# Kernel tuning notes

Hardware: AMD Instinct MI355X
Metric: run time of the kernel (lower is better)

The kernel has to match this reference:

```python
import jax, jax.numpy as jnp
import numpy as np

N, A, B, C = 256, 1024, 64, 16


def setup_inputs() -> dict:
    key = jax.random.key(0)
    k1, k2, k3 = jax.random.split(key, 3)
    x = jax.random.normal(k1, (N, A), dtype=jnp.float32)
    weight = jax.random.normal(k2, (A, B * C), dtype=jnp.float32) * 0.02
    bias = jax.random.normal(k3, (B,), dtype=jnp.float32) * 0.02
    return {"x": x, "weight": weight, "bias": bias}


def reference(x, weight, bias):
    # x: [N, A]; weight: [A, B*C]; bias: [B]
    n = x.shape[0]
    mat = (x @ weight).reshape(n, B, C)              # [N, B, C]
    # pairwise L1 over the C (kernel) axis -> [N, N, B]
    l1 = jnp.abs(mat[:, None, :, :] - mat[None, :, :, :]).sum(axis=-1)
    # exp(-L1), sum over the first (broadcast) axis as in the torch code,
    # which includes the self term exp(0)=1
    out = jnp.exp(-l1).sum(axis=0) + bias            # [N, B]
    return out
```

## Files before the change

### kernel.cpp

```cpp
#include <hip/hip_runtime.h>

#define LOG2E 1.4426950408889634f

typedef __bf16 bf16x8 __attribute__((ext_vector_type(8)));
typedef float  f32x4  __attribute__((ext_vector_type(4)));

__device__ inline unsigned short f2bf(float f){
  unsigned u = __float_as_uint(f);
  unsigned r = u + 0x7FFFu + ((u >> 16) & 1u);
  return (unsigned short)(r >> 16);
}
__device__ inline unsigned pack2(float lo, float hi){
  return (unsigned)f2bf(lo) | ((unsigned)f2bf(hi) << 16);
}

__global__ __launch_bounds__(256) void k_gemm_fused(const float* __restrict__ X,
                                                    const float* __restrict__ Wm,
                                                    float* __restrict__ mat){
  __shared__ unsigned short As[64 * 72];
  __shared__ unsigned short Bs[64 * 72];
  const int m0 = blockIdx.x * 64, n0 = blockIdx.y * 64;
  const int t = threadIdx.x;
  const int lane = t & 63, w = t >> 6;
  const int wrow = (w & 1) * 32, wcol = (w >> 1) * 32;
  const int r16 = lane & 15, quad = lane >> 4;

  const int ar = t >> 2, aq = t & 3;
  const int bc = t & 15, bg = t >> 4;
  const float* ap = X + (size_t)(m0 + ar) * 1024 + aq * 16;
  const float* bp = Wm + n0 + bc * 4;

  f32x4 acc[2][2];
  #pragma unroll
  for (int p = 0; p < 2; ++p)
    #pragma unroll
    for (int q = 0; q < 2; ++q)
      #pragma unroll
      for (int e = 0; e < 4; ++e) acc[p][q][e] = 0.f;

  float4 pa[4], pb[4];
  #pragma unroll
  for (int r = 0; r < 4; ++r) pa[r] = *(const float4*)(ap + r * 4);
  #pragma unroll
  for (int r = 0; r < 4; ++r) pb[r] = *(const float4*)(bp + (size_t)(4 * bg + r) * 1024);

  for (int kt = 0; kt < 1024; kt += 64){
    __syncthreads();
    {
      unsigned short* d = &As[ar * 72 + aq * 16];
      uint4 o;
      o.x = pack2(pa[0].x, pa[0].y); o.y = pack2(pa[0].z, pa[0].w);
      o.z = pack2(pa[1].x, pa[1].y); o.w = pack2(pa[1].z, pa[1].w);
      *(uint4*)d = o;
      o.x = pack2(pa[2].x, pa[2].y); o.y = pack2(pa[2].z, pa[2].w);
      o.z = pack2(pa[3].x, pa[3].y); o.w = pack2(pa[3].z, pa[3].w);
      *(uint4*)(d + 8) = o;
    }
    {
      #pragma unroll
      for (int e = 0; e < 4; ++e){
        const int n = bc * 4 + e;
        uint2 o;
        o.x = pack2(((const float*)&pb[0])[e], ((const float*)&pb[1])[e]);
        o.y = pack2(((const float*)&pb[2])[e], ((const float*)&pb[3])[e]);
        const int cw = (bg >> 1) ^ ((n >> 3) & 7);
        *(uint2*)(&Bs[n * 72 + cw * 8 + (bg & 1) * 4]) = o;
      }
    }
    __syncthreads();
    if (kt + 64 < 1024){
      #pragma unroll
      for (int r = 0; r < 4; ++r) pa[r] = *(const float4*)(ap + kt + 64 + r * 4);
      #pragma unroll
      for (int r = 0; r < 4; ++r) pb[r] = *(const float4*)(bp + (size_t)(kt + 64 + 4 * bg + r) * 1024);
    }
    #pragma unroll
    for (int kk = 0; kk < 2; ++kk){
      const int ko = kk * 32 + quad * 8;
      bf16x8 a0 = *(const bf16x8*)(&As[(wrow      + r16) * 72 + ko]);
      bf16x8 a1 = *(const bf16x8*)(&As[(wrow + 16 + r16) * 72 + ko]);
      const int c = kk * 4 + quad;
      const int nb0 = wcol + r16, nb1 = wcol + 16 + r16;
      bf16x8 b0 = *(const bf16x8*)(&Bs[nb0 * 72 + ((c ^ ((nb0 >> 3) & 7)) * 8)]);
      bf16x8 b1 = *(const bf16x8*)(&Bs[nb1 * 72 + ((c ^ ((nb1 >> 3) & 7)) * 8)]);
      acc[0][0] = __builtin_amdgcn_mfma_f32_16x16x32_bf16(a0, b0, acc[0][0], 0, 0, 0);
      acc[0][1] = __builtin_amdgcn_mfma_f32_16x16x32_bf16(a0, b1, acc[0][1], 0, 0, 0);
      acc[1][0] = __builtin_amdgcn_mfma_f32_16x16x32_bf16(a1, b0, acc[1][0], 0, 0, 0);
      acc[1][1] = __builtin_amdgcn_mfma_f32_16x16x32_bf16(a1, b1, acc[1][1], 0, 0, 0);
    }
  }
  #pragma unroll
  for (int p = 0; p < 2; ++p)
    #pragma unroll
    for (int q = 0; q < 2; ++q)
      #pragma unroll
      for (int r = 0; r < 4; ++r){
        const int row = m0 + wrow + p * 16 + quad * 4 + r;
        const int col = n0 + wcol + q * 16 + r16;
        mat[(size_t)row * 1024 + col] = acc[p][q][r];
      }
}

__global__ __launch_bounds__(512) void k_pair(const float* __restrict__ mat,
                                              const float* __restrict__ bias,
                                              float* __restrict__ out){
  __shared__ float L[256 * 16];
  __shared__ float red[8][64];
  const int b = blockIdx.x >> 2, jc = blockIdx.x & 3;
  const int t = threadIdx.x, lane = t & 63, w = t >> 6;

  #pragma unroll
  for (int p = 0; p < 2; ++p){
    const int f = t + p * 512;
    const int i = f >> 2, q = f & 3;
    *(float4*)(&L[i * 16 + q * 4]) =
        *(const float4*)(mat + (size_t)i * 1024 + b * 16 + q * 4);
  }
  __syncthreads();

  const int j = jc * 64 + lane;
  float oj[16];
  #pragma unroll
  for (int q = 0; q < 4; ++q){
    float4 v = *(const float4*)(&L[j * 16 + q * 4]);
    oj[q*4+0] = v.x; oj[q*4+1] = v.y; oj[q*4+2] = v.z; oj[q*4+3] = v.w;
  }

  float acc = 0.f;
  const int i0 = w * 32;
  for (int ii = i0; ii < i0 + 32; ++ii){
    const float4* fr = (const float4*)(&L[ii * 16]);
    float4 f0 = fr[0], f1 = fr[1], f2 = fr[2], f3 = fr[3];
    float p0 = fabsf(oj[0]  - f0.x) + fabsf(oj[1]  - f0.y)
             + fabsf(oj[2]  - f0.z) + fabsf(oj[3]  - f0.w);
    float p1 = fabsf(oj[4]  - f1.x) + fabsf(oj[5]  - f1.y)
             + fabsf(oj[6]  - f1.z) + fabsf(oj[7]  - f1.w);
    float p2 = fabsf(oj[8]  - f2.x) + fabsf(oj[9]  - f2.y)
             + fabsf(oj[10] - f2.z) + fabsf(oj[11] - f2.w);
    float p3 = fabsf(oj[12] - f3.x) + fabsf(oj[13] - f3.y)
             + fabsf(oj[14] - f3.z) + fabsf(oj[15] - f3.w);
    acc += exp2f(-LOG2E * ((p0 + p1) + (p2 + p3)));
  }
  red[w][lane] = acc;
  __syncthreads();
  if (w == 0){
    float tot = 0.f;
    #pragma unroll
    for (int ww = 0; ww < 8; ++ww) tot += red[ww][lane];
    out[(size_t)j * 64 + b] = tot + bias[b];
  }
}

extern "C" void kernel_launch(void* const* d_in, const int* in_sizes, int n_in,
                              void* d_out, int out_size, void* d_ws, size_t ws_size,
                              hipStream_t stream){
  const float* x    = (const float*)d_in[0];
  const float* W    = (const float*)d_in[1];
  const float* bias = (const float*)d_in[2];
  float* out = (float*)d_out;
  float* mat = (float*)d_ws;

  k_gemm_fused<<<dim3(4, 16), 256, 0, stream>>>(x, W, mat);
  k_pair<<<256, 512, 0, stream>>>(mat, bias, out);
}
```

Before: 83.35 us.

## Split GEMM along K into four partials and reduce them in pair kernel

The GEMM grid gains a K-split dimension, so 256 blocks each compute a quarter of the K range and write partial products to separate workspace slices. The pair kernel sums the four partials while loading its tile into shared memory. It also doubles its block size to 1024 threads so each wave handles fewer rows. The intent is to fill the GPU with more GEMM blocks instead of 64 long-running ones, at the cost of four times the workspace traffic and a larger reduction in the pair kernel.

```diff
diff --git a/kernel.cpp b/kernel.cpp
--- a/kernel.cpp
+++ b/kernel.cpp
@@ -14,12 +14,13 @@
   return (unsigned)f2bf(lo) | ((unsigned)f2bf(hi) << 16);
 }
 
-__global__ __launch_bounds__(256) void k_gemm_fused(const float* __restrict__ X,
-                                                    const float* __restrict__ Wm,
-                                                    float* __restrict__ mat){
+__global__ __launch_bounds__(256) void k_gemm_ks(const float* __restrict__ X,
+                                                 const float* __restrict__ Wm,
+                                                 float* __restrict__ P){
   __shared__ unsigned short As[64 * 72];
   __shared__ unsigned short Bs[64 * 72];
   const int m0 = blockIdx.x * 64, n0 = blockIdx.y * 64;
+  const int k0 = blockIdx.z * 256;
   const int t = threadIdx.x;
   const int lane = t & 63, w = t >> 6;
   const int wrow = (w & 1) * 32, wcol = (w >> 1) * 32;
@@ -27,8 +28,8 @@
 
   const int ar = t >> 2, aq = t & 3;
   const int bc = t & 15, bg = t >> 4;
-  const float* ap = X + (size_t)(m0 + ar) * 1024 + aq * 16;
-  const float* bp = Wm + n0 + bc * 4;
+  const float* ap = X + (size_t)(m0 + ar) * 1024 + k0 + aq * 16;
+  const float* bp = Wm + (size_t)k0 * 1024 + n0 + bc * 4;
 
   f32x4 acc[2][2];
   #pragma unroll
@@ -44,7 +45,8 @@
   #pragma unroll
   for (int r = 0; r < 4; ++r) pb[r] = *(const float4*)(bp + (size_t)(4 * bg + r) * 1024);
 
-  for (int kt = 0; kt < 1024; kt += 64){
+  #pragma unroll
+  for (int kt = 0; kt < 256; kt += 64){
     __syncthreads();
     {
       unsigned short* d = &As[ar * 72 + aq * 16];
@@ -68,7 +70,7 @@
       }
     }
     __syncthreads();
-    if (kt + 64 < 1024){
+    if (kt < 192){
       #pragma unroll
       for (int r = 0; r < 4; ++r) pa[r] = *(const float4*)(ap + kt + 64 + r * 4);
       #pragma unroll
@@ -89,6 +91,7 @@
       acc[1][1] = __builtin_amdgcn_mfma_f32_16x16x32_bf16(a1, b1, acc[1][1], 0, 0, 0);
     }
   }
+  float* Pz = P + (size_t)blockIdx.z * 256 * 1024;
   #pragma unroll
   for (int p = 0; p < 2; ++p)
     #pragma unroll
@@ -97,24 +100,31 @@
       for (int r = 0; r < 4; ++r){
         const int row = m0 + wrow + p * 16 + quad * 4 + r;
         const int col = n0 + wcol + q * 16 + r16;
-        mat[(size_t)row * 1024 + col] = acc[p][q][r];
+        Pz[(size_t)row * 1024 + col] = acc[p][q][r];
       }
 }
 
-__global__ __launch_bounds__(512) void k_pair(const float* __restrict__ mat,
-                                              const float* __restrict__ bias,
-                                              float* __restrict__ out){
+__global__ __launch_bounds__(1024) void k_pair(const float* __restrict__ P,
+                                               const float* __restrict__ bias,
+                                               float* __restrict__ out){
   __shared__ float L[256 * 16];
-  __shared__ float red[8][64];
+  __shared__ float red[16][64];
   const int b = blockIdx.x >> 2, jc = blockIdx.x & 3;
   const int t = threadIdx.x, lane = t & 63, w = t >> 6;
 
-  #pragma unroll
-  for (int p = 0; p < 2; ++p){
-    const int f = t + p * 512;
-    const int i = f >> 2, q = f & 3;
-    *(float4*)(&L[i * 16 + q * 4]) =
-        *(const float4*)(mat + (size_t)i * 1024 + b * 16 + q * 4);
+  {
+    const int i = t >> 2, q = t & 3;
+    const float* base = P + (size_t)i * 1024 + b * 16 + q * 4;
+    float4 s0 = *(const float4*)(base);
+    float4 s1 = *(const float4*)(base + 256 * 1024);
+    float4 s2 = *(const float4*)(base + 512 * 1024);
+    float4 s3 = *(const float4*)(base + 768 * 1024);
+    float4 r;
+    r.x = (s0.x + s1.x) + (s2.x + s3.x);
+    r.y = (s0.y + s1.y) + (s2.y + s3.y);
+    r.z = (s0.z + s1.z) + (s2.z + s3.z);
+    r.w = (s0.w + s1.w) + (s2.w + s3.w);
+    *(float4*)(&L[i * 16 + q * 4]) = r;
   }
   __syncthreads();
 
@@ -127,8 +137,9 @@
   }
 
   float acc = 0.f;
-  const int i0 = w * 32;
-  for (int ii = i0; ii < i0 + 32; ++ii){
+  const int i0 = w * 16;
+  #pragma unroll 4
+  for (int ii = i0; ii < i0 + 16; ++ii){
     const float4* fr = (const float4*)(&L[ii * 16]);
     float4 f0 = fr[0], f1 = fr[1], f2 = fr[2], f3 = fr[3];
     float p0 = fabsf(oj[0]  - f0.x) + fabsf(oj[1]  - f0.y)
@@ -146,7 +157,7 @@
   if (w == 0){
     float tot = 0.f;
     #pragma unroll
-    for (int ww = 0; ww < 8; ++ww) tot += red[ww][lane];
+    for (int ww = 0; ww < 16; ++ww) tot += red[ww][lane];
     out[(size_t)j * 64 + b] = tot + bias[b];
   }
 }
@@ -158,8 +169,8 @@
   const float* W    = (const float*)d_in[1];
   const float* bias = (const float*)d_in[2];
   float* out = (float*)d_out;
-  float* mat = (float*)d_ws;
+  float* P   = (float*)d_ws;
 
-  k_gemm_fused<<<dim3(4, 16), 256, 0, stream>>>(x, W, mat);
-  k_pair<<<256, 512, 0, stream>>>(mat, bias, out);
+  k_gemm_ks<<<dim3(4, 16, 4), 256, 0, stream>>>(x, W, P);
+  k_pair<<<256, 1024, 0, stream>>>(P, bias, out);
 }
```

Result: faster. 76.73 us (-7.9%).
